# Performance work log

Measured on AMD Instinct MI355X. Metric: run time of the kernel, lower is better.

## Reference

```python
import jax, jax.numpy as jnp
import numpy as np
from jax import lax

LOG2PI = 1.8378770664093453


def _lstm_last(x, Wih, Whh, b, reverse):
    # x: [N, T, D]; returns hidden output at the LAST timestep index (torch output[:, -1])
    N = x.shape[0]
    H = Whh.shape[1]
    xg = jnp.einsum('ntd,gd->tng', x, Wih) + b  # [T, N, 4H], gate order i,f,g,o

    def step(carry, g_in):
        h, c = carry
        g = g_in + h @ Whh.T
        i, f, gg, o = jnp.split(g, 4, axis=-1)
        c = jax.nn.sigmoid(f) * c + jax.nn.sigmoid(i) * jnp.tanh(gg)
        h = jax.nn.sigmoid(o) * jnp.tanh(c)
        return (h, c), h

    init = (jnp.zeros((N, H), x.dtype), jnp.zeros((N, H), x.dtype))
    _, hs = lax.scan(step, init, xg, reverse=reverse)
    return hs[-1]  # fw: full pass; bw(reverse=True): processed only last element, as torch


def _dvbf(x, u, eps1, eps, fw_Wih, fw_Whh, fw_b, bw_Wih, bw_Whh, bw_b,
          i1_w, i1_b, i2_w, i2_b, z1_w, z1_b, z2_w, z2_b,
          wp_w1, wp_b1, wp_w2, wp_b2, vp_w1, vp_b1, vp_w2, vp_b2,
          ob_w1, ob_b1, ob_w2, ob_b2, A, B, C):
    N, T, dx = x.shape
    dw = eps1.shape[1]
    # initial samples from bidirectional LSTM output at t = T-1 (fw || bw)
    h0 = jnp.concatenate([_lstm_last(x, fw_Wih, fw_Whh, fw_b, False),
                          _lstm_last(x, bw_Wih, bw_Whh, bw_b, True)], axis=1)
    p0 = jax.nn.relu(h0 @ i1_w.T + i1_b) @ i2_w.T + i2_b
    m0, s0_raw = jnp.split(p0, 2, axis=1)
    s0 = jnp.exp(s0_raw) + 1e-5
    w1 = m0 + s0 * eps1  # reparameterized torch.normal(mean, std)
    z1 = jax.nn.relu(w1 @ z1_w.T + z1_b) @ z2_w.T + z2_b

    def step(z_t, inp):
        x_t, u_t, e_t = inp
        pw = jnp.tanh(jnp.concatenate([x_t, z_t, u_t], axis=1) @ wp_w1.T + wp_b1) @ wp_w2.T + wp_b2
        m, s_raw = jnp.split(pw, 2, axis=1)
        s = jnp.exp(s_raw) + 0.01
        w_t = m + s * e_t
        alpha = jax.nn.softmax(
            jax.nn.relu(jnp.concatenate([z_t, u_t], axis=1) @ vp_w1.T + vp_b1) @ vp_w2.T + vp_b2,
            axis=1)
        z_n = (jnp.einsum('nm,mij,nj->ni', alpha, A, z_t)
               + jnp.einsum('nm,mij,nj->ni', alpha, B, u_t)
               + jnp.einsum('nm,mij,nj->ni', alpha, C, w_t))
        return z_n, (z_n, m, s)

    xs = (jnp.swapaxes(x[:, 1:], 0, 1), jnp.swapaxes(u[:, :T - 1], 0, 1), jnp.swapaxes(eps[:, 1:], 0, 1))
    _, (zs, ms, ss) = lax.scan(step, z1, xs)
    z = jnp.concatenate([z1[:, None], jnp.swapaxes(zs, 0, 1)], axis=1)        # [N,T,dz]
    w_mean = jnp.concatenate([m0[:, None], jnp.swapaxes(ms, 0, 1)], axis=1)   # [N,T,dw]
    w_std = jnp.concatenate([s0[:, None], jnp.swapaxes(ss, 0, 1)], axis=1)

    x_rec = jax.nn.relu(z @ ob_w1.T + ob_b1) @ ob_w2.T + ob_b2                # [N,T,dx]
    logprob_x = -0.5 * jnp.sum((x - x_rec) ** 2) - 0.5 * N * T * dx * LOG2PI
    # KL(N(m, diag(std)) || N(0, I)) -- the module uses std as the covariance diagonal
    kl = 0.5 * (jnp.sum(w_std) + jnp.sum(w_mean ** 2) - N * T * dw - jnp.sum(jnp.log(w_std)))
    return -(logprob_x - kl)


def setup_inputs() -> dict:
    key = jax.random.key(0)
    ks = iter(jax.random.split(key, 64))

    def rn(shape, s=1.0):
        return s * jax.random.normal(next(ks), shape, dtype=jnp.float32)

    N, T, DX, DU, DZ, DW, M, H = 512, 128, 256, 32, 128, 64, 16, 128
    S = 0.05  # weight scale keeps the recurrence stable
    return {
        'x': rn((N, T, DX)), 'u': rn((N, T, DU)),
        'eps1': rn((N, DW)), 'eps': rn((N, T, DW)),
        'fw_Wih': rn((4 * H, DX), S), 'fw_Whh': rn((4 * H, H), S), 'fw_b': rn((4 * H,), S),
        'bw_Wih': rn((4 * H, DX), S), 'bw_Whh': rn((4 * H, H), S), 'bw_b': rn((4 * H,), S),
        'i1_w': rn((H, 2 * H), S), 'i1_b': rn((H,), S), 'i2_w': rn((2 * DW, H), S), 'i2_b': rn((2 * DW,), S),
        'z1_w': rn((H, DW), S), 'z1_b': rn((H,), S), 'z2_w': rn((DZ, H), S), 'z2_b': rn((DZ,), S),
        'wp_w1': rn((H, DZ + DU + DX), S), 'wp_b1': rn((H,), S), 'wp_w2': rn((2 * DW, H), S), 'wp_b2': rn((2 * DW,), S),
        'vp_w1': rn((H, DZ + DU), S), 'vp_b1': rn((H,), S), 'vp_w2': rn((M, H), S), 'vp_b2': rn((M,), S),
        'ob_w1': rn((H, DZ), S), 'ob_b1': rn((H,), S), 'ob_w2': rn((DX, H), S), 'ob_b2': rn((DX,), S),
        'A': rn((M, DZ, DZ), S), 'B': rn((M, DZ, DU), S), 'C': rn((M, DZ, DW), S),
    }


def reference(x, u, eps1, eps, fw_Wih, fw_Whh, fw_b, bw_Wih, bw_Whh, bw_b,
              i1_w, i1_b, i2_w, i2_b, z1_w, z1_b, z2_w, z2_b,
              wp_w1, wp_b1, wp_w2, wp_b2, vp_w1, vp_b1, vp_w2, vp_b2,
              ob_w1, ob_b1, ob_w2, ob_b2, A, B, C):
    return _dvbf(x, u, eps1, eps, fw_Wih, fw_Whh, fw_b, bw_Wih, bw_Whh, bw_b,
                 i1_w, i1_b, i2_w, i2_b, z1_w, z1_b, z2_w, z2_b,
                 wp_w1, wp_b1, wp_w2, wp_b2, vp_w1, vp_b1, vp_w2, vp_b2,
                 ob_w1, ob_b1, ob_w2, ob_b2, A, B, C)
```

## Files before the change

kernel.cpp:

```cpp
#include <hip/hip_runtime.h>
#include <stdint.h>
#include <math.h>

#define NB  512
#define TT  128
#define DXX 256
#define DUU 32
#define DZZ 128
#define DWW 64
#define MMM 16
#define HHH 128
#define G4  512

typedef __attribute__((ext_vector_type(8))) short bf16x8;
typedef __attribute__((ext_vector_type(4))) float f32x4;
#define MFMA(a,b,c) __builtin_amdgcn_mfma_f32_16x16x32_bf16(a,b,c,0,0,0)
#define MF8(a,b,c)  __builtin_amdgcn_mfma_f32_16x16x32_fp8_fp8(a,b,c,0,0,0)

__device__ __forceinline__ float sigf(float x){ return 1.f/(1.f+__expf(-x)); }
__device__ __forceinline__ float fast_tanh(float x){
    float e = __expf(2.f*x);
    return 1.f - 2.f/(e + 1.f);
}
__device__ __forceinline__ unsigned int f2bf(float f){
// ... 23 lines not shown
        if (rs >= 33) return s;
        uint64_t full = (uint64_t)(mant | 0x800000u);
        uint64_t q = full >> rs;
        uint64_t rem = full & (((uint64_t)1 << rs) - 1);
        uint64_t half = (uint64_t)1 << (rs - 1);
        if (rem > half || (rem == half && (q & 1))) q++;
        code = (uint32_t)q;
    }
    return s | code;
}

__device__ __forceinline__ void stage1k(const void* gsrc, void* ldst, int ln)
{
    __builtin_amdgcn_global_load_lds(
        (const __attribute__((address_space(1))) void*)((const char*)gsrc + ln*16),
        (__attribute__((address_space(3))) void*)ldst, 16, 0, 0);
}
__device__ __forceinline__ void stage32k(const void* gsrc, void* ldst, int tid)
{
    const char* g = (const char*)gsrc;
    char* l = (char*)ldst;
    const int lane = tid & 63;
    const int wv   = tid >> 6;
    #pragma unroll
    for (int it = 0; it < 8; it++){
        const int off = it*4096 + wv*1024;
        __builtin_amdgcn_global_load_lds(
            (const __attribute__((address_space(1))) void*)(g + off + lane*16),
            (__attribute__((address_space(3))) void*)(l + off),
            16, 0, 0);
    }
}

__global__ __launch_bounds__(256) void k_prep2(
    const float* __restrict__ wp_w1, const float* __restrict__ wp_w2,
    const float* __restrict__ vp_w1, const float* __restrict__ vp_w2,
    unsigned short* __restrict__ frag)
{
    const int T = blockIdx.x;
    unsigned short* dst = frag + (size_t)T*512;
    for (int e = threadIdx.x; e < 512; e += 256){
        const int lane = e >> 3, j = e & 7;
        const int m16 = lane & 15, kq = lane >> 4;
        const int kk = 8*kq + j;
        float v = 0.f;
        if (T < 104){
            const int ct = T/13, kt = T%13;
            v = wp_w1[(size_t)(16*ct + m16)*416 + 32*kt + kk];
        } else if (T < 136){
            const int i = T-104, ct = i/4, kt = i%4;
            v = wp_w2[(size_t)(16*ct + m16)*128 + 32*kt + kk];
        } else if (T < 176){
            const int i = T-136, ct = i/5, kt = i%5;
            v = vp_w1[(size_t)(16*ct + m16)*160 + 32*kt + kk];
        } else {
            const int kt = T-176;
            v = vp_w2[(size_t)m16*128 + 32*kt + kk];
        }
        dst[e] = (unsigned short)f2bf(v);
    }
}

__global__ __launch_bounds__(256) void k_prep8(
    const float* __restrict__ Amat, const float* __restrict__ Bmat,
    const float* __restrict__ Cmat, unsigned char* __restrict__ frag8)
{
    const int wv = blockIdx.x >> 3, pair = blockIdx.x & 7;
    unsigned char* dst = frag8 + (size_t)blockIdx.x*7168;
    for (int d = threadIdx.x*4; d < 7168; d += 1024){
        uint32_t pk = 0;
        #pragma unroll
        for (int i = 0; i < 4; i++){
            const int B = d + i;
            const int f = B >> 9, r = B & 511;
            const int lane = r >> 3, jj = r & 7;
            const int m = 2*pair + (f >= 7 ? 1 : 0);
            const int kt = (f >= 7) ? f-7 : f;
            const int col = wv*16 + (lane & 15);
            const int k = kt*32 + (lane >> 4)*8 + jj;
            float v;
            if (k < 128)      v = Amat[((size_t)m*128 + col)*128 + k];
            else if (k < 160) v = Bmat[((size_t)m*128 + col)*32 + (k-128)];
            else              v = Cmat[((size_t)m*128 + col)*64 + (k-160)];
            pk |= f2e4m3(v * 16.f) << (8*i);
        }
        *(uint32_t*)(dst + d) = pk;
    }
}

__global__ __launch_bounds__(256) void k_prep_xg(const float* __restrict__ Wih,
                                                 unsigned short* __restrict__ fragx)
{
    const int T = blockIdx.x;
    const int ct = T >> 3, kt = T & 7;
    unsigned short* dst = fragx + (size_t)T*512;
    for (int e = threadIdx.x; e < 512; e += 256){
        const int lane = e >> 3, j = e & 7;
        const int m16 = lane & 15, kq = lane >> 4;
        const int kk = 8*kq + j;
        float v = Wih[(size_t)(16*ct + m16)*DXX + 32*kt + kk];
        dst[e] = (unsigned short)f2bf(v);
    }
}

__global__ __launch_bounds__(256) void k_prep_lo(
    const float* __restrict__ Whh,
    const float* __restrict__ ob_w1, const float* __restrict__ ob_w2,
    unsigned short* __restrict__ blstm, unsigned short* __restrict__ bob)
{
    const int tile = blockIdx.x;
    unsigned short* dst; int lt;
    if (tile < 4){ dst = blstm + (size_t)tile*16384; lt = 1; }
    else { dst = bob + (size_t)(tile-4)*16384; lt = 2; }
    for (int e = threadIdx.x; e < 16384; e += 256){
        const int g = e >> 7, p = e & 127;
        const int s = p >> 3, j = p & 7;
        const int k = ((s ^ (g & 7)) << 3) | j;
        float v;
        if (lt == 1) v = Whh[(size_t)(tile*128 + g)*128 + k];
        else {
            const int tt = tile - 4;
            if (tt == 0) v = ob_w1[g*128 + k];
            else         v = ob_w2[(size_t)((tt-1)*128 + g)*128 + k];
        }
        dst[e] = (unsigned short)f2bf(v);
    }
}

__global__ __launch_bounds__(256) void k_prep_in(
    const float* __restrict__ X, const float* __restrict__ U, const float* __restrict__ EPS,
    unsigned short* __restrict__ IX, unsigned short* __restrict__ IU,
    unsigned short* __restrict__ IE, unsigned char* __restrict__ IUf)
{
    const int b  = blockIdx.x;
    const int tt = blockIdx.y;
    const int n0 = b*16;
    unsigned short* dx = IX + ((size_t)b*127 + tt)*4096;
    for (int h = threadIdx.x; h < 4096; h += 256){
        const int o = h >> 9, l = (h >> 3) & 63, j = h & 7;
        const int r = 2*o + (l >> 5), v = l & 31;
        const int s = v ^ (r & 7);
        dx[h] = (unsigned short)f2bf(X[((size_t)(n0+r)*TT + tt+1)*DXX + s*8 + j]);
    }
    unsigned short* du = IU + ((size_t)b*127 + tt)*512;
    for (int h = threadIdx.x; h < 512; h += 256){
        const int l = h >> 3, j = h & 7;
        const int r = l >> 2, v = l & 3;
        const int qq = v ^ (r & 3);
        du[h] = (unsigned short)f2bf(U[((size_t)(n0+r)*TT + tt)*DUU + qq*8 + j]);
    }
    unsigned short* de = IE + ((size_t)b*127 + tt)*1024;
    for (int h = threadIdx.x; h < 1024; h += 256){
        const int e2 = h >> 9, l = (h >> 3) & 63, j = h & 7;
        const int r = 8*e2 + (l >> 3);
        de[h] = (unsigned short)f2bf(EPS[((size_t)(n0+r)*TT + tt+1)*DWW + (l&7)*8 + j]);
    }
    unsigned char* df = IUf + ((size_t)b*127 + tt)*512;
    for (int h = threadIdx.x; h < 512; h += 256){
        const int smp = h >> 5, sp = (h >> 3) & 3, j = h & 7;
        const int ud = ((sp ^ (smp & 3))*8) + j;
        df[h] = (unsigned char)f2e4m3(U[((size_t)(n0+smp)*TT + tt)*DUU + ud]);
    }
}

template<int ACT>
__device__ void dense(const float* __restrict__ W, const float* __restrict__ bias,
                      int C, int K, const float* sIn, int ldi,
                      float* sOut, int ldo, float* sWt)
{
    const int tid = threadIdx.x;
    const int g   = tid & 127;
    const int rq  = tid >> 7;
    const int r0  = 2*rq, r1 = 2*rq+1;
    for (int cb = 0; cb < C; cb += 128){
        float acc0 = 0.f, acc1 = 0.f;
        for (int kb = 0; kb < K; kb += 64){
            const int kw = (K - kb < 64) ? (K - kb) : 64;
            __syncthreads();
            if (kw == 64){
                for (int l = tid; l < 128*64; l += 256){
                    int gg = l >> 6, kk = l & 63;
                    int cx = cb + gg;
                    sWt[gg*65 + kk] = (cx < C) ? W[(size_t)cx*K + kb + kk] : 0.f;
                }
            } else {
                for (int l = tid; l < 128*32; l += 256){
                    int gg = l >> 5, kk = l & 31;
                    int cx = cb + gg;
                    sWt[gg*65 + kk] = (cx < C) ? W[(size_t)cx*K + kb + kk] : 0.f;
                }
            }
            __syncthreads();
            const float* ip0 = sIn + r0*ldi + kb;
            const float* ip1 = sIn + r1*ldi + kb;
            const float* wp  = sWt + g*65;
// ... 140 lines not shown
        sH0[r*260+j] = h0[(size_t)(n0+r)*HHH + j];
    }
    dense<0>(bw_Wih, bw_b, 512, 256, sX, 260, sG, 516, sWt);
    __syncthreads();
    for (int l = tid; l < 4*128; l += 256){
        int r = l >> 7, j = l & 127;
        float gi = sG[r*516 + j];
        float gv = sG[r*516 + 256 + j];
        float go = sG[r*516 + 384 + j];
        float c  = sigf(gi)*fast_tanh(gv);
        sH0[r*260 + 128 + j] = sigf(go)*fast_tanh(c);
    }
    dense<1>(i1w, i1b, 128, 256, sH0, 260, sT, 132, sWt);
    dense<0>(i2w, i2b, 128, 128, sT, 132, sP, 132, sWt);
    __syncthreads();
    for (int l = tid; l < 4*64; l += 256){
        int r = l >> 6, j = l & 63;
        float m0 = sP[r*132 + j];
        float s0 = __expf(sP[r*132 + 64 + j]) + 1e-5f;
        float w1 = m0 + s0*eps1[(size_t)(n0+r)*DWW + j];
        wm[((size_t)(n0+r)*TT)*DWW + j]  = m0;
        wsd[((size_t)(n0+r)*TT)*DWW + j] = s0;
        sX[r*68 + j] = w1;
    }
    dense<1>(z1w, z1b, 128, 64, sX, 68, sT, 132, sWt);
    dense<0>(z2w, z2b, 128, 128, sT, 132, sP, 132, sWt);
    __syncthreads();
    for (int l = tid; l < 4*128; l += 256){
        int r = l >> 7, j = l & 127;
        zb[((size_t)(n0+r)*TT)*DZZ + j] = sP[r*132+j];
    }
}

__device__ __forceinline__ int blobIdx(int i, int wv){
    if (i < 13)  return wv*13 + i;
    if (i < 18)  return 136 + wv*5 + (i-13);
    if (i < 22)  return 104 + wv*4 + (i-18);
    if (i < 26)  return 176 + (i-22);
    return 0;
}

#define VWAIT() do{ asm volatile("s_waitcnt vmcnt(7)" ::: "memory"); \
                    __builtin_amdgcn_sched_barrier(0); }while(0)
#define LWAIT() do{ asm volatile("s_waitcnt lgkmcnt(0)" ::: "memory"); \
                    __builtin_amdgcn_sched_barrier(0); }while(0)
#define BAR()   __builtin_amdgcn_s_barrier()

__global__ __launch_bounds__(512) void k_scan(
    const float* __restrict__ wp_b1, const float* __restrict__ wp_b2,
    const float* __restrict__ vp_b1, const float* __restrict__ vp_b2,
    const short* __restrict__ frag, const unsigned char* __restrict__ frag8,
    const unsigned short* __restrict__ IX, const unsigned short* __restrict__ IU,
    const unsigned short* __restrict__ IE, const unsigned char* __restrict__ IUf,
    float* __restrict__ zb, float* __restrict__ wm, float* __restrict__ wsd)
{
    __shared__ __align__(16) short sRing[57344];
    __shared__ __align__(16) short sXr[4096];
    __shared__ __align__(16) short sZr[2048];
    __shared__ __align__(16) short sUr[2][512];
    __shared__ __align__(16) short sEr[1024];
    __shared__ __align__(16) short sH1[2048];
    __shared__ __align__(16) short sH2[2048];
    __shared__ __align__(16) char  sZf[2048];
    __shared__ __align__(16) char  sUf[2][512];
    __shared__ __align__(16) char  sWf[1024];
    __shared__ __align__(16) float sPW[16*132];
    __shared__ __align__(16) float sL [16*20];
    __shared__ float sAl[16*17];

    const int tid = threadIdx.x;
    const int n0  = blockIdx.x * 16;
    const int wv  = tid >> 6;
    const int ln  = tid & 63;
    const int smp = ln & 15, q = ln >> 4;
    const int sx7 = smp & 7;
    char* ringB = (char*)sRing + wv*14336;

    const f32x4 bw1 = *(const f32x4*)&wp_b1[wv*16 + q*4];
    const f32x4 bw2 = *(const f32x4*)&wp_b2[wv*16 + q*4];
    const f32x4 bv1 = *(const f32x4*)&vp_b1[wv*16 + q*4];
    f32x4 bv2 = {0.f,0.f,0.f,0.f};
    if (wv == 0) bv2 = *(const f32x4*)&vp_b2[q*4];

    #define ISSUE_CHUNK(cc_) do{ const int c2_ = (cc_) % 12; \
        if (c2_ < 4){ _Pragma("unroll") \
            for (int k7 = 0; k7 < 7; k7++) \
                stage1k((const char*)frag + (size_t)blobIdx(c2_*7 + k7, wv)*1024, \
                        ringB + (c2_&1)*7168 + k7*1024, ln); \
        } else { _Pragma("unroll") \
            for (int k7 = 0; k7 < 7; k7++) \
                stage1k((const char*)frag8 + (size_t)(wv*8 + (c2_-4))*7168 + k7*1024, \
                        ringB + (c2_&1)*7168 + k7*1024, ln); } }while(0)
    #define AFRAG(gi_)  (*(const bf16x8*)(ringB + (((gi_)/7)&1)*7168 + ((gi_)%7)*1024 + ln*16))
    #define AF8(bf_,f_) (*(const long*)(ringB + (bf_)*7168 + (f_)*512 + ln*8))
    #define BX(kt_)  (*(const bf16x8*)&sXr[smp*256 + (((4*(kt_)+q) ^ sx7)<<3)])
    #define BZ(kz_)  (*(const bf16x8*)&sZr[smp*128 + (((4*(kz_)+q) ^ sx7)<<3)])
    #define BH1(kt_) (*(const bf16x8*)&sH1[smp*128 + (((4*(kt_)+q) ^ sx7)<<3)])
    #define BH2(kt_) (*(const bf16x8*)&sH2[smp*128 + (((4*(kt_)+q) ^ sx7)<<3)])

    auto issue_inputs = [&](int tt){
        const size_t ib = (size_t)blockIdx.x*127 + tt;
        const char* bx8 = (const char*)IX + ib*8192;
        stage1k(bx8 + wv*1024, (char*)sXr + wv*1024, ln);
        if (wv == 0)      stage1k((const char*)IU + ib*1024, (char*)sUr[tt&1], ln);
        else if (wv == 1) stage1k((const char*)IE + ib*2048,        (char*)sEr,        ln);
        else if (wv == 2) stage1k((const char*)IE + ib*2048 + 1024, (char*)sEr + 1024, ln);
        else if (wv == 3){ if (ln < 32) stage1k((const char*)IUf + ib*512, sUf[tt&1], ln); }
    };

    issue_inputs(0);
    if (tid < 256){
        const int zs = tid >> 4, sl = tid & 15;
        const float* zp = &zb[((size_t)(n0+zs)*TT)*DZZ + sl*8];
        float4 a0 = *(const float4*)zp;
        float4 a1 = *(const float4*)(zp+4);
        int4 pk;
        pk.x = f2bf(a0.x) | (f2bf(a0.y)<<16);
        pk.y = f2bf(a0.z) | (f2bf(a0.w)<<16);
        pk.z = f2bf(a1.x) | (f2bf(a1.y)<<16);
        pk.w = f2bf(a1.z) | (f2bf(a1.w)<<16);
        *(int4*)&sZr[zs*128 + ((sl ^ (zs&7))<<3)] = pk;
        uint2 p8;
        p8.x = f2e4m3(a0.x) | (f2e4m3(a0.y)<<8) | (f2e4m3(a0.z)<<16) | (f2e4m3(a0.w)<<24);
        p8.y = f2e4m3(a1.x) | (f2e4m3(a1.y)<<8) | (f2e4m3(a1.z)<<16) | (f2e4m3(a1.w)<<24);
        *(uint2*)&sZf[zs*128 + ((sl ^ (zs&7))<<3)] = p8;
    }
    ISSUE_CHUNK(0);
    ISSUE_CHUNK(1);
    asm volatile("s_waitcnt vmcnt(0)" ::: "memory");
    __builtin_amdgcn_sched_barrier(0);
    LWAIT(); BAR();

    for (int t = 0; t < TT-1; t++){
        const short* sUc = sUr[t&1];
        bf16x8 bu = *(const bf16x8*)&sUc[smp*32 + ((q ^ (sx7&3))<<3)];

        VWAIT();
        f32x4 d1a = {0.f,0.f,0.f,0.f}, d1b = {0.f,0.f,0.f,0.f};
        d1a = MFMA(AFRAG(0), BX(0), d1a); d1b = MFMA(AFRAG(1), BX(1), d1b);
        d1a = MFMA(AFRAG(2), BX(2), d1a); d1b = MFMA(AFRAG(3), BX(3), d1b);
        d1a = MFMA(AFRAG(4), BX(4), d1a); d1b = MFMA(AFRAG(5), BX(5), d1b);
        d1a = MFMA(AFRAG(6), BX(6), d1a);
        ISSUE_CHUNK(2);
        VWAIT();
        d1b = MFMA(AFRAG(7), BX(7), d1b);
        d1a = MFMA(AFRAG(8), BZ(0), d1a); d1b = MFMA(AFRAG(9), BZ(1), d1b);
        d1a = MFMA(AFRAG(10), BZ(2), d1a); d1b = MFMA(AFRAG(11), BZ(3), d1b);
        d1a = MFMA(AFRAG(12), bu, d1a);
        f32x4 d3a = {0.f,0.f,0.f,0.f}, d3b = {0.f,0.f,0.f,0.f};
        d3a = MFMA(AFRAG(13), BZ(0), d3a);
        ISSUE_CHUNK(3);
        VWAIT();
        d3b = MFMA(AFRAG(14), BZ(1), d3b); d3a = MFMA(AFRAG(15), BZ(2), d3a);
        d3b = MFMA(AFRAG(16), BZ(3), d3b); d3a = MFMA(AFRAG(17), bu, d3a);
        bf16x8 aG2a = AFRAG(18), aG2b = AFRAG(19), aG2c = AFRAG(20);
        {
            f32x4 d1 = d1a + d1b, d3 = d3a + d3b;
            float v0 = fast_tanh(d1[0]+bw1[0]);
            float v1 = fast_tanh(d1[1]+bw1[1]);
            float v2 = fast_tanh(d1[2]+bw1[2]);
            float v3 = fast_tanh(d1[3]+bw1[3]);
            const int slot = 2*wv + (q>>1);
            const int baseh = smp*128 + ((slot ^ sx7)<<3) + (q&1)*4;
            *(unsigned int*)&sH1[baseh]   = f2bf(v0) | (f2bf(v1)<<16);
            *(unsigned int*)&sH1[baseh+2] = f2bf(v2) | (f2bf(v3)<<16);
            float w0 = fmaxf(d3[0]+bv1[0], 0.f);
            float w1 = fmaxf(d3[1]+bv1[1], 0.f);
            float w2 = fmaxf(d3[2]+bv1[2], 0.f);
            float w3 = fmaxf(d3[3]+bv1[3], 0.f);
            *(unsigned int*)&sH2[baseh]   = f2bf(w0) | (f2bf(w1)<<16);
            *(unsigned int*)&sH2[baseh+2] = f2bf(w2) | (f2bf(w3)<<16);
        }
        ISSUE_CHUNK(4);
        LWAIT(); BAR();

        VWAIT();
        {
            f32x4 d2a = {0.f,0.f,0.f,0.f}, d2b = {0.f,0.f,0.f,0.f};
            d2a = MFMA(aG2a, BH1(0), d2a); d2b = MFMA(aG2b, BH1(1), d2b);
            d2a = MFMA(aG2c, BH1(2), d2a); d2b = MFMA(AFRAG(21), BH1(3), d2b);
            f32x4 o = d2a + d2b + bw2;
            *(f32x4*)&sPW[smp*132 + wv*16 + q*4] = o;
            if (wv == 0){
                f32x4 d4a = {0.f,0.f,0.f,0.f}, d4b = {0.f,0.f,0.f,0.f};
                d4a = MFMA(AFRAG(22), BH2(0), d4a); d4b = MFMA(AFRAG(23), BH2(1), d4b);
                d4a = MFMA(AFRAG(24), BH2(2), d4a); d4b = MFMA(AFRAG(25), BH2(3), d4b);
                f32x4 o4 = d4a + d4b + bv2;
                *(f32x4*)&sL[smp*20 + q*4] = o4;
            }
        }
        ISSUE_CHUNK(5);
        LWAIT(); BAR();

        {
            const int cs = wv, cj = ln;
            float e0 = bf2f((unsigned short)sEr[cs*64 + cj]);
            float e1 = bf2f((unsigned short)sEr[(cs+8)*64 + cj]);
            float m0 = sPW[cs*132 + cj];
            float s0 = __expf(sPW[cs*132 + 64 + cj]) + 0.01f;
            float m1 = sPW[(cs+8)*132 + cj];
            float s1 = __expf(sPW[(cs+8)*132 + 64 + cj]) + 0.01f;
            float w0 = m0 + s0*e0;
            float w1 = m1 + s1*e1;
            wm [((size_t)(n0+cs  )*TT + t+1)*DWW + cj] = m0;
            wsd[((size_t)(n0+cs  )*TT + t+1)*DWW + cj] = s0;
            wm [((size_t)(n0+cs+8)*TT + t+1)*DWW + cj] = m1;
            wsd[((size_t)(n0+cs+8)*TT + t+1)*DWW + cj] = s1;
            const int sw = cj >> 3;
            sWf[ cs   *64 + ((sw ^ ( cs   &7))<<3) + (cj&7)] = (char)f2e4m3(w0);
            sWf[(cs+8)*64 + ((sw ^ ((cs+8)&7))<<3) + (cj&7)] = (char)f2e4m3(w1);
        }
        if (tid < 16){
            float mx = -1e30f;
            #pragma unroll
            for (int m = 0; m < 16; m++) mx = fmaxf(mx, sL[tid*20+m]);
            float ss = 0.f;
            float ex[16];
            #pragma unroll
            for (int m = 0; m < 16; m++){ ex[m] = __expf(sL[tid*20+m]-mx); ss += ex[m]; }
            float inv = 0.0625f/ss;
            #pragma unroll
            for (int m = 0; m < 16; m++) sAl[tid*17+m] = ex[m]*inv;
        }
        if (t < TT-2) issue_inputs(t+1);
        LWAIT(); BAR();

        long bz0 = *(const long*)&sZf[smp*128 + (((0*4+q) ^ sx7)<<3)];
        long bz1 = *(const long*)&sZf[smp*128 + (((1*4+q) ^ sx7)<<3)];
        long bz2 = *(const long*)&sZf[smp*128 + (((2*4+q) ^ sx7)<<3)];
        long bz3 = *(const long*)&sZf[smp*128 + (((3*4+q) ^ sx7)<<3)];
        long bu8 = *(const long*)&sUf[t&1][smp*32 + ((q ^ (smp&3))<<3)];
        long bw80 = *(const long*)&sWf[smp*64 + ((q ^ sx7)<<3)];
        long bw81 = *(const long*)&sWf[smp*64 + (((4+q) ^ sx7)<<3)];
        f32x4 zac = {0.f,0.f,0.f,0.f};
        #pragma unroll
        for (int j = 0; j < 8; j++){
            const int bf = j & 1;
            VWAIT();
            f32x4 d = {0.f,0.f,0.f,0.f}, e = {0.f,0.f,0.f,0.f};
            d = MF8(AF8(bf,0), bz0, d); e = MF8(AF8(bf,1), bz1, e);
            d = MF8(AF8(bf,2), bz2, d); e = MF8(AF8(bf,3), bz3, e);
            d = MF8(AF8(bf,4), bu8, d); e = MF8(AF8(bf,5), bw80, e);
            d = MF8(AF8(bf,6), bw81, d);
            f32x4 g = {0.f,0.f,0.f,0.f}, h = {0.f,0.f,0.f,0.f};
            g = MF8(AF8(bf,7), bz0, g);  h = MF8(AF8(bf,8), bz1, h);
            g = MF8(AF8(bf,9), bz2, g);  h = MF8(AF8(bf,10), bz3, h);
            g = MF8(AF8(bf,11), bu8, g); h = MF8(AF8(bf,12), bw80, h);
            g = MF8(AF8(bf,13), bw81, g);
            ISSUE_CHUNK(6+j);
            const float al0 = sAl[smp*17 + 2*j];
            const float al1 = sAl[smp*17 + 2*j + 1];
            f32x4 s0 = d + e, s1 = g + h;
            zac[0] += al0*s0[0] + al1*s1[0];
            zac[1] += al0*s0[1] + al1*s1[1];
            zac[2] += al0*s0[2] + al1*s1[2];
            zac[3] += al0*s0[3] + al1*s1[3];
        }
        LWAIT(); BAR();

        {
            const int slotz = 2*wv + (q>>1);
            const int basez = smp*128 + ((slotz ^ sx7)<<3) + (q&1)*4;
            *(unsigned int*)&sZr[basez]   = f2bf(zac[0]) | (f2bf(zac[1])<<16);
            *(unsigned int*)&sZr[basez+2] = f2bf(zac[2]) | (f2bf(zac[3])<<16);
            unsigned int p8 = f2e4m3(zac[0]) | (f2e4m3(zac[1])<<8)
                            | (f2e4m3(zac[2])<<16) | (f2e4m3(zac[3])<<24);
            *(unsigned int*)&sZf[smp*128 + ((slotz ^ sx7)<<3) + (q&1)*4] = p8;
            float4 st = {zac[0], zac[1], zac[2], zac[3]};
            *(float4*)&zb[((size_t)(n0+smp)*TT + t+1)*DZZ + wv*16 + q*4] = st;
        }
        LWAIT(); BAR();
    }
    asm volatile("s_waitcnt vmcnt(0) lgkmcnt(0)" ::: "memory");
    #undef ISSUE_CHUNK
    #undef AFRAG
    #undef AF8
    #undef BX
    #undef BZ
    #undef BH1
    #undef BH2
}

__global__ __launch_bounds__(256) void k_ob(const float* __restrict__ X,
        const float* __restrict__ zb,
        const float* __restrict__ b1, const float* __restrict__ b2,
        const unsigned short* __restrict__ blob, float* __restrict__ acc)
{
    __shared__ __align__(16) char  sW[2][32768];
    __shared__ __align__(16) float sZ[32*128];
    __shared__ __align__(16) float sH[32*128];
    __shared__ float redb[4];
    const int tid = threadIdx.x;
    const size_t row0 = (size_t)blockIdx.x * 32;
    const int g = tid & 127, rh = tid >> 7;
    for (int l = tid; l < 32*128; l += 256)
        sZ[l] = zb[(row0 + (size_t)(l >> 7))*DZZ + (l & 127)];
    stage32k((const char*)blob, sW[0], tid);
    asm volatile("s_waitcnt vmcnt(0)" ::: "memory");
    __syncthreads();
    stage32k((const char*)blob + 32768, sW[1], tid);
    float h[16];
    #pragma unroll
    for (int r = 0; r < 16; r++) h[r] = 0.f;
    #pragma unroll 4
    for (int s = 0; s < 16; s++){
        const uint32_t* wp = (const uint32_t*)(sW[0] + g*256 + ((s ^ (g & 7)) << 4));
        float wv[8];
        #pragma unroll
        for (int d = 0; d < 4; d++){
            uint32_t w2 = wp[d];
            wv[2*d]   = __uint_as_float(w2 << 16);
            wv[2*d+1] = __uint_as_float(w2 & 0xffff0000u);
        }
// ... 114 lines not shown
    const float* i1w = (const float*)d_in[10];
    const float* i1b = (const float*)d_in[11];
    const float* i2w = (const float*)d_in[12];
    const float* i2b = (const float*)d_in[13];
    const float* z1w = (const float*)d_in[14];
    const float* z1b = (const float*)d_in[15];
    const float* z2w = (const float*)d_in[16];
    const float* z2b = (const float*)d_in[17];
    const float* wp_w1 = (const float*)d_in[18];
    const float* wp_b1 = (const float*)d_in[19];
    const float* wp_w2 = (const float*)d_in[20];
    const float* wp_b2 = (const float*)d_in[21];
    const float* vp_w1 = (const float*)d_in[22];
    const float* vp_b1 = (const float*)d_in[23];
    const float* vp_w2 = (const float*)d_in[24];
    const float* vp_b2 = (const float*)d_in[25];
    const float* ob_w1 = (const float*)d_in[26];
    const float* ob_b1 = (const float*)d_in[27];
    const float* ob_w2 = (const float*)d_in[28];
    const float* ob_b2 = (const float*)d_in[29];
    const float* Amat  = (const float*)d_in[30];
    const float* Bmat  = (const float*)d_in[31];
    const float* Cmat  = (const float*)d_in[32];
    float* out = (float*)d_out;

    unsigned short* xgb = (unsigned short*)d_ws;
    float* h0  = (float*)(xgb + (size_t)NB*TT*G4);
    float* zb  = h0  + (size_t)NB*HHH;
    float* wm  = zb  + (size_t)NB*TT*DZZ;
    float* wsd = wm  + (size_t)NB*TT*DWW;
    float* acc = wsd + (size_t)NB*TT*DWW;
    unsigned short* blstm = (unsigned short*)(acc + 64);
    unsigned short* bob   = blstm + (size_t)4*16384;
    unsigned short* bfrag = bob   + (size_t)3*16384;
    unsigned short* bfragx= bfrag + (size_t)180*512;
    unsigned char*  bfrag8= (unsigned char*)(bfragx + (size_t)256*512);
    unsigned short* IX    = (unsigned short*)(bfrag8 + (size_t)64*7168);
    unsigned short* IU    = IX + (size_t)32*127*4096;
    unsigned short* IE    = IU + (size_t)32*127*512;
    unsigned char*  IUf   = (unsigned char*)(IE + (size_t)32*127*1024);

    hipMemsetAsync(acc, 0, 4*sizeof(float), stream);

    k_prep2<<<180, 256, 0, stream>>>(wp_w1, wp_w2, vp_w1, vp_w2, bfrag);
    k_prep8<<<64, 256, 0, stream>>>(Amat, Bmat, Cmat, bfrag8);
    k_prep_xg<<<256, 256, 0, stream>>>(fw_Wih, bfragx);
    k_prep_lo<<<7, 256, 0, stream>>>(fw_Whh, ob_w1, ob_w2, blstm, bob);
    k_prep_in<<<dim3(32,127), 256, 0, stream>>>(x, u, eps, IX, IU, IE, IUf);
    k_xg2 <<<NB*TT/16, 512, 0, stream>>>(x, bfragx, fw_b, xgb);
    k_lstm<<<NB/2, 256, 0, stream>>>(xgb, blstm, h0);
    k_init<<<NB/4, 256, 0, stream>>>(x, bw_Wih, bw_b, i1w, i1b, i2w, i2b,
                                     z1w, z1b, z2w, z2b, eps1, h0, zb, wm, wsd);
    k_scan<<<32, 512, 0, stream>>>(wp_b1, wp_b2, vp_b1, vp_b2,
                                   (const short*)bfrag, bfrag8, IX, IU, IE, IUf,
                                   zb, wm, wsd);
    k_ob  <<<NB*TT/32, 256, 0, stream>>>(x, zb, ob_b1, ob_b2, bob, acc);
    k_kl  <<<NB*TT*DWW/4096, 256, 0, stream>>>(wm, wsd, acc);
    k_final<<<1, 64, 0, stream>>>(acc, out);
}
```

Before: 2.941 ms.

## Precompute x/u projections outside the scan and run all recurrent matmuls in fp8

The input-dependent parts of the first layers of the wp and vp MLPs (x and u terms plus biases) are now computed for every timestep in a new parallel kernel before the scan. The sequential scan keeps only the z-dependent projections, and those, along with the second layers, now use fp8 MFMA with a scaling factor instead of bf16. A single fp8 weight blob per wave is streamed through a larger LDS ring in 8 KB chunks, which removes the bf16/fp8 split and the X staging. The aim is to shorten the serial critical path of the scan. The cost is extra workspace traffic and lower precision in the hidden activations, which are now quantised to e4m3.

```diff
diff --git a/kernel.cpp b/kernel.cpp
--- a/kernel.cpp
+++ b/kernel.cpp
@@ -79,59 +79,56 @@
     }
 }
 
-__global__ __launch_bounds__(256) void k_prep2(
+__global__ __launch_bounds__(256) void k_prep8b(
     const float* __restrict__ wp_w1, const float* __restrict__ wp_w2,
     const float* __restrict__ vp_w1, const float* __restrict__ vp_w2,
-    unsigned short* __restrict__ frag)
-{
-    const int T = blockIdx.x;
-    unsigned short* dst = frag + (size_t)T*512;
+    const float* __restrict__ Amat,  const float* __restrict__ Bmat,
+    const float* __restrict__ Cmat,  unsigned char* __restrict__ frag8)
+{
+    const int wv = blockIdx.x >> 3, c = blockIdx.x & 7;
+    unsigned char* dst = frag8 + (size_t)(wv*8 + c)*8192;
+    for (int d = threadIdx.x*4; d < 8192; d += 1024){
+        uint32_t pk = 0;
+        #pragma unroll
+        for (int i = 0; i < 4; i++){
+            const int B = d + i;
+            const int f = 16*c + (B >> 9), r = B & 511;
+            const int lane = r >> 3, jj = r & 7;
+            const int col = wv*16 + (lane & 15);
+            const int kk = (lane >> 4)*8 + jj;
+            float v = 0.f;
+            if (f < 4)       v = wp_w1[(size_t)col*416 + 256 + f*32 + kk];
+            else if (f < 8)  v = vp_w1[(size_t)col*160 + (f-4)*32 + kk];
+            else if (f < 12) v = wp_w2[(size_t)col*128 + (f-8)*32 + kk];
+            else if (f < 16){ if (wv == 0) v = vp_w2[(size_t)(col&15)*128 + (f-12)*32 + kk]; }
+            else {
+                const int fi = f-16, m = fi/7, kt = fi%7;
+                const int k = kt*32 + kk;
+                if (k < 128)      v = Amat[((size_t)m*128 + col)*128 + k];
+                else if (k < 160) v = Bmat[((size_t)m*128 + col)*32 + (k-128)];
+                else              v = Cmat[((size_t)m*128 + col)*64 + (k-160)];
+            }
+            pk |= f2e4m3(v * 16.f) << (8*i);
+        }
+        *(uint32_t*)(dst + d) = pk;
+    }
+}
+
+__global__ __launch_bounds__(256) void k_prep_p(
+    const float* __restrict__ wp_w1, const float* __restrict__ vp_w1,
+    unsigned short* __restrict__ fragP)
+{
+    const int ct = blockIdx.x / 10, f = blockIdx.x % 10;
+    unsigned short* dst = fragP + (size_t)blockIdx.x*512;
     for (int e = threadIdx.x; e < 512; e += 256){
         const int lane = e >> 3, j = e & 7;
-        const int m16 = lane & 15, kq = lane >> 4;
-        const int kk = 8*kq + j;
-        float v = 0.f;
-        if (T < 104){
-            const int ct = T/13, kt = T%13;
-            v = wp_w1[(size_t)(16*ct + m16)*416 + 32*kt + kk];
-        } else if (T < 136){
-            const int i = T-104, ct = i/4, kt = i%4;
-            v = wp_w2[(size_t)(16*ct + m16)*128 + 32*kt + kk];
-        } else if (T < 176){
-            const int i = T-136, ct = i/5, kt = i%5;
-            v = vp_w1[(size_t)(16*ct + m16)*160 + 32*kt + kk];
-        } else {
-            const int kt = T-176;
-            v = vp_w2[(size_t)m16*128 + 32*kt + kk];
-        }
+        const int col = 16*ct + (lane & 15);
+        const int kk = (lane >> 4)*8 + j;
+        float v;
+        if (f < 8)      v = wp_w1[(size_t)col*416 + f*32 + kk];
+        else if (f == 8) v = wp_w1[(size_t)col*416 + 384 + kk];
+        else             v = vp_w1[(size_t)col*160 + 128 + kk];
         dst[e] = (unsigned short)f2bf(v);
-    }
-}
-
-__global__ __launch_bounds__(256) void k_prep8(
-    const float* __restrict__ Amat, const float* __restrict__ Bmat,
-    const float* __restrict__ Cmat, unsigned char* __restrict__ frag8)
-{
-    const int wv = blockIdx.x >> 3, pair = blockIdx.x & 7;
-    unsigned char* dst = frag8 + (size_t)blockIdx.x*7168;
-    for (int d = threadIdx.x*4; d < 7168; d += 1024){
-        uint32_t pk = 0;
-        #pragma unroll
-        for (int i = 0; i < 4; i++){
-            const int B = d + i;
-            const int f = B >> 9, r = B & 511;
-            const int lane = r >> 3, jj = r & 7;
-            const int m = 2*pair + (f >= 7 ? 1 : 0);
-            const int kt = (f >= 7) ? f-7 : f;
-            const int col = wv*16 + (lane & 15);
-            const int k = kt*32 + (lane >> 4)*8 + jj;
-            float v;
-            if (k < 128)      v = Amat[((size_t)m*128 + col)*128 + k];
-            else if (k < 160) v = Bmat[((size_t)m*128 + col)*32 + (k-128)];
-            else              v = Cmat[((size_t)m*128 + col)*64 + (k-160)];
-            pk |= f2e4m3(v * 16.f) << (8*i);
-        }
-        *(uint32_t*)(dst + d) = pk;
     }
 }
 
@@ -175,27 +172,12 @@
 }
 
 __global__ __launch_bounds__(256) void k_prep_in(
-    const float* __restrict__ X, const float* __restrict__ U, const float* __restrict__ EPS,
-    unsigned short* __restrict__ IX, unsigned short* __restrict__ IU,
+    const float* __restrict__ U, const float* __restrict__ EPS,
     unsigned short* __restrict__ IE, unsigned char* __restrict__ IUf)
 {
     const int b  = blockIdx.x;
     const int tt = blockIdx.y;
     const int n0 = b*16;
-    unsigned short* dx = IX + ((size_t)b*127 + tt)*4096;
-    for (int h = threadIdx.x; h < 4096; h += 256){
-        const int o = h >> 9, l = (h >> 3) & 63, j = h & 7;
-        const int r = 2*o + (l >> 5), v = l & 31;
-        const int s = v ^ (r & 7);
-        dx[h] = (unsigned short)f2bf(X[((size_t)(n0+r)*TT + tt+1)*DXX + s*8 + j]);
-    }
-    unsigned short* du = IU + ((size_t)b*127 + tt)*512;
-    for (int h = threadIdx.x; h < 512; h += 256){
-        const int l = h >> 3, j = h & 7;
-        const int r = l >> 2, v = l & 3;
-        const int qq = v ^ (r & 3);
-        du[h] = (unsigned short)f2bf(U[((size_t)(n0+r)*TT + tt)*DUU + qq*8 + j]);
-    }
     unsigned short* de = IE + ((size_t)b*127 + tt)*1024;
     for (int h = threadIdx.x; h < 1024; h += 256){
         const int e2 = h >> 9, l = (h >> 3) & 63, j = h & 7;
@@ -208,6 +190,65 @@
         const int ud = ((sp ^ (smp & 3))*8) + j;
         df[h] = (unsigned char)f2e4m3(U[((size_t)(n0+smp)*TT + tt)*DUU + ud]);
     }
+}
+
+__global__ __launch_bounds__(512) void k_pxu(
+    const float* __restrict__ X, const float* __restrict__ U,
+    const float* __restrict__ wp_b1, const float* __restrict__ vp_b1,
+    const unsigned short* __restrict__ fragP,
+    unsigned short* __restrict__ IPx, unsigned short* __restrict__ IPL)
+{
+    __shared__ __align__(16) short sXl[16*256];
+    __shared__ __align__(16) short sUl[16*32];
+    const int tid = threadIdx.x;
+    const int b = blockIdx.x, t = blockIdx.y;
+    const int n0 = b*16;
+    const int wv = tid >> 6, ln = tid & 63;
+    const int rr = ln & 15, q = ln >> 4;
+    const int sx7 = rr & 7;
+    {
+        const int r = tid >> 5, sl = tid & 31;
+        const float* xp = &X[((size_t)(n0+r)*TT + t+1)*DXX + sl*8];
+        float4 a0 = *(const float4*)xp;
+        float4 a1 = *(const float4*)(xp+4);
+        int4 pk;
+        pk.x = f2bf(a0.x) | (f2bf(a0.y)<<16);
+        pk.y = f2bf(a0.z) | (f2bf(a0.w)<<16);
+        pk.z = f2bf(a1.x) | (f2bf(a1.y)<<16);
+        pk.w = f2bf(a1.z) | (f2bf(a1.w)<<16);
+        *(int4*)&sXl[r*256 + ((sl ^ (r&7))<<3)] = pk;
+    }
+    {
+        const int r = tid >> 5, cc = tid & 31;
+        sUl[r*32 + (((cc>>3) ^ (r&3))<<3) + (cc&7)] =
+            (unsigned short)f2bf(U[((size_t)(n0+r)*TT + t)*DUU + cc]);
+    }
+    __syncthreads();
+    const short* pA = (const short*)fragP + (size_t)wv*10*512 + ln*8;
+    f32x4 d = {0.f,0.f,0.f,0.f};
+    #pragma unroll
+    for (int kt = 0; kt < 8; kt++){
+        bf16x8 a = *(const bf16x8*)(pA + kt*512);
+        bf16x8 bx = *(const bf16x8*)&sXl[rr*256 + (((4*kt+q) ^ sx7)<<3)];
+        d = MFMA(a, bx, d);
+    }
+    bf16x8 bu = *(const bf16x8*)&sUl[rr*32 + ((q ^ (rr&3))<<3)];
+    d = MFMA(*(const bf16x8*)(pA + 8*512), bu, d);
+    f32x4 dl = {0.f,0.f,0.f,0.f};
+    dl = MFMA(*(const bf16x8*)(pA + 9*512), bu, dl);
+    const f32x4 b1v = *(const f32x4*)&wp_b1[wv*16 + q*4];
+    const f32x4 bLv = *(const f32x4*)&vp_b1[wv*16 + q*4];
+    d = d + b1v;
+    dl = dl + bLv;
+    const size_t base = ((size_t)b*127 + t)*2048
+                      + rr*128 + (((2*wv + (q>>1)) ^ sx7)<<3) + (q&1)*4;
+    uint2 p1, p2;
+    p1.x = f2bf(d[0]) | (f2bf(d[1])<<16);
+    p1.y = f2bf(d[2]) | (f2bf(d[3])<<16);
+    p2.x = f2bf(dl[0]) | (f2bf(dl[1])<<16);
+    p2.y = f2bf(dl[2]) | (f2bf(dl[3])<<16);
+    *(uint2*)&IPx[base] = p1;
+    *(uint2*)&IPL[base] = p2;
 }
 
 template<int ACT>
@@ -414,38 +455,28 @@
     }
 }
 
-__device__ __forceinline__ int blobIdx(int i, int wv){
-    if (i < 13)  return wv*13 + i;
-    if (i < 18)  return 136 + wv*5 + (i-13);
-    if (i < 22)  return 104 + wv*4 + (i-18);
-    if (i < 26)  return 176 + (i-22);
-    return 0;
-}
-
-#define VWAIT() do{ asm volatile("s_waitcnt vmcnt(7)" ::: "memory"); \
+#define VWAIT8() do{ asm volatile("s_waitcnt vmcnt(8)" ::: "memory"); \
                     __builtin_amdgcn_sched_barrier(0); }while(0)
 #define LWAIT() do{ asm volatile("s_waitcnt lgkmcnt(0)" ::: "memory"); \
                     __builtin_amdgcn_sched_barrier(0); }while(0)
 #define BAR()   __builtin_amdgcn_s_barrier()
 
 __global__ __launch_bounds__(512) void k_scan(
-    const float* __restrict__ wp_b1, const float* __restrict__ wp_b2,
-    const float* __restrict__ vp_b1, const float* __restrict__ vp_b2,
-    const short* __restrict__ frag, const unsigned char* __restrict__ frag8,
-    const unsigned short* __restrict__ IX, const unsigned short* __restrict__ IU,
+    const float* __restrict__ wp_b2, const float* __restrict__ vp_b2,
+    const unsigned char* __restrict__ frag8,
+    const unsigned short* __restrict__ IPx, const unsigned short* __restrict__ IPL,
     const unsigned short* __restrict__ IE, const unsigned char* __restrict__ IUf,
     float* __restrict__ zb, float* __restrict__ wm, float* __restrict__ wsd)
 {
-    __shared__ __align__(16) short sRing[57344];
-    __shared__ __align__(16) short sXr[4096];
-    __shared__ __align__(16) short sZr[2048];
-    __shared__ __align__(16) short sUr[2][512];
-    __shared__ __align__(16) short sEr[1024];
-    __shared__ __align__(16) short sH1[2048];
-    __shared__ __align__(16) short sH2[2048];
+    __shared__ __align__(16) short sRing[65536];
+    __shared__ __align__(16) short sPx[2048];
+    __shared__ __align__(16) short sPL[2048];
     __shared__ __align__(16) char  sZf[2048];
     __shared__ __align__(16) char  sUf[2][512];
     __shared__ __align__(16) char  sWf[1024];
+    __shared__ __align__(16) short sEr[1024];
+    __shared__ __align__(16) char  sH1f[2048];
+    __shared__ __align__(16) char  sH2f[2048];
     __shared__ __align__(16) float sPW[16*132];
     __shared__ __align__(16) float sL [16*20];
     __shared__ float sAl[16*17];
@@ -456,38 +487,29 @@
     const int ln  = tid & 63;
     const int smp = ln & 15, q = ln >> 4;
     const int sx7 = smp & 7;
-    char* ringB = (char*)sRing + wv*14336;
-
-    const f32x4 bw1 = *(const f32x4*)&wp_b1[wv*16 + q*4];
+    char* ringB = (char*)sRing + wv*16384;
+    const unsigned char* myblob = frag8 + (size_t)wv*65536;
+
     const f32x4 bw2 = *(const f32x4*)&wp_b2[wv*16 + q*4];
-    const f32x4 bv1 = *(const f32x4*)&vp_b1[wv*16 + q*4];
     f32x4 bv2 = {0.f,0.f,0.f,0.f};
     if (wv == 0) bv2 = *(const f32x4*)&vp_b2[q*4];
 
-    #define ISSUE_CHUNK(cc_) do{ const int c2_ = (cc_) % 12; \
-        if (c2_ < 4){ _Pragma("unroll") \
-            for (int k7 = 0; k7 < 7; k7++) \
-                stage1k((const char*)frag + (size_t)blobIdx(c2_*7 + k7, wv)*1024, \
-                        ringB + (c2_&1)*7168 + k7*1024, ln); \
-        } else { _Pragma("unroll") \
-            for (int k7 = 0; k7 < 7; k7++) \
-                stage1k((const char*)frag8 + (size_t)(wv*8 + (c2_-4))*7168 + k7*1024, \
-                        ringB + (c2_&1)*7168 + k7*1024, ln); } }while(0)
-    #define AFRAG(gi_)  (*(const bf16x8*)(ringB + (((gi_)/7)&1)*7168 + ((gi_)%7)*1024 + ln*16))
-    #define AF8(bf_,f_) (*(const long*)(ringB + (bf_)*7168 + (f_)*512 + ln*8))
-    #define BX(kt_)  (*(const bf16x8*)&sXr[smp*256 + (((4*(kt_)+q) ^ sx7)<<3)])
-    #define BZ(kz_)  (*(const bf16x8*)&sZr[smp*128 + (((4*(kz_)+q) ^ sx7)<<3)])
-    #define BH1(kt_) (*(const bf16x8*)&sH1[smp*128 + (((4*(kt_)+q) ^ sx7)<<3)])
-    #define BH2(kt_) (*(const bf16x8*)&sH2[smp*128 + (((4*(kt_)+q) ^ sx7)<<3)])
+    #define ISSUE_CHUNK(cc_) do{ const int c2_ = (cc_) & 7; \
+        _Pragma("unroll") \
+        for (int k8 = 0; k8 < 8; k8++) \
+            stage1k(myblob + (size_t)c2_*8192 + k8*1024, \
+                    ringB + (c2_&1)*8192 + k8*1024, ln); }while(0)
+    #define AF8(f_) (*(const long*)(ringB + (((f_)>>4)&1)*8192 + ((f_)&15)*512 + ln*8))
+    #define BH1F(t_) (*(const long*)&sH1f[smp*128 + (((4*(t_)+q) ^ sx7)<<3)])
+    #define BH2F(t_) (*(const long*)&sH2f[smp*128 + (((4*(t_)+q) ^ sx7)<<3)])
 
     auto issue_inputs = [&](int tt){
         const size_t ib = (size_t)blockIdx.x*127 + tt;
-        const char* bx8 = (const char*)IX + ib*8192;
-        stage1k(bx8 + wv*1024, (char*)sXr + wv*1024, ln);
-        if (wv == 0)      stage1k((const char*)IU + ib*1024, (char*)sUr[tt&1], ln);
-        else if (wv == 1) stage1k((const char*)IE + ib*2048,        (char*)sEr,        ln);
-        else if (wv == 2) stage1k((const char*)IE + ib*2048 + 1024, (char*)sEr + 1024, ln);
-        else if (wv == 3){ if (ln < 32) stage1k((const char*)IUf + ib*512, sUf[tt&1], ln); }
+        if (wv < 4) stage1k((const char*)IPx + ib*4096 + wv*1024, (char*)sPx + wv*1024, ln);
+        else        stage1k((const char*)IPL + ib*4096 + (wv-4)*1024, (char*)sPL + (wv-4)*1024, ln);
+        if (wv == 0)      stage1k((const char*)IE + ib*2048,        (char*)sEr,        ln);
+        else if (wv == 1) stage1k((const char*)IE + ib*2048 + 1024, (char*)sEr + 1024, ln);
+        else if (wv == 2){ if (ln < 32) stage1k((const char*)IUf + ib*512, sUf[tt&1], ln); }
     };
 
     issue_inputs(0);
@@ -496,12 +518,6 @@
         const float* zp = &zb[((size_t)(n0+zs)*TT)*DZZ + sl*8];
         float4 a0 = *(const float4*)zp;
         float4 a1 = *(const float4*)(zp+4);
-        int4 pk;
-        pk.x = f2bf(a0.x) | (f2bf(a0.y)<<16);
-        pk.y = f2bf(a0.z) | (f2bf(a0.w)<<16);
-        pk.z = f2bf(a1.x) | (f2bf(a1.y)<<16);
-        pk.w = f2bf(a1.z) | (f2bf(a1.w)<<16);
-        *(int4*)&sZr[zs*128 + ((sl ^ (zs&7))<<3)] = pk;
         uint2 p8;
         p8.x = f2e4m3(a0.x) | (f2e4m3(a0.y)<<8) | (f2e4m3(a0.z)<<16) | (f2e4m3(a0.w)<<24);
         p8.y = f2e4m3(a1.x) | (f2e4m3(a1.y)<<8) | (f2e4m3(a1.z)<<16) | (f2e4m3(a1.w)<<24);
@@ -514,64 +530,57 @@
     LWAIT(); BAR();
 
     for (int t = 0; t < TT-1; t++){
-        const short* sUc = sUr[t&1];
-        bf16x8 bu = *(const bf16x8*)&sUc[smp*32 + ((q ^ (sx7&3))<<3)];
-
-        VWAIT();
+        long bz0 = *(const long*)&sZf[smp*128 + (((0*4+q) ^ sx7)<<3)];
+        long bz1 = *(const long*)&sZf[smp*128 + (((1*4+q) ^ sx7)<<3)];
+        long bz2 = *(const long*)&sZf[smp*128 + (((2*4+q) ^ sx7)<<3)];
+        long bz3 = *(const long*)&sZf[smp*128 + (((3*4+q) ^ sx7)<<3)];
+
+        VWAIT8();
         f32x4 d1a = {0.f,0.f,0.f,0.f}, d1b = {0.f,0.f,0.f,0.f};
-        d1a = MFMA(AFRAG(0), BX(0), d1a); d1b = MFMA(AFRAG(1), BX(1), d1b);
-        d1a = MFMA(AFRAG(2), BX(2), d1a); d1b = MFMA(AFRAG(3), BX(3), d1b);
-        d1a = MFMA(AFRAG(4), BX(4), d1a); d1b = MFMA(AFRAG(5), BX(5), d1b);
-        d1a = MFMA(AFRAG(6), BX(6), d1a);
+        d1a = MF8(AF8(0), bz0, d1a); d1b = MF8(AF8(1), bz1, d1b);
+        d1a = MF8(AF8(2), bz2, d1a); d1b = MF8(AF8(3), bz3, d1b);
+        f32x4 d3a = {0.f,0.f,0.f,0.f}, d3b = {0.f,0.f,0.f,0.f};
+        d3a = MF8(AF8(4), bz0, d3a); d3b = MF8(AF8(5), bz1, d3b);
+        d3a = MF8(AF8(6), bz2, d3a); d3b = MF8(AF8(7), bz3, d3b);
+        long aG2_0 = AF8(8),  aG2_1 = AF8(9),  aG2_2 = AF8(10), aG2_3 = AF8(11);
+        long aG4_0 = AF8(12), aG4_1 = AF8(13), aG4_2 = AF8(14), aG4_3 = AF8(15);
+        LWAIT();
         ISSUE_CHUNK(2);
-        VWAIT();
-        d1b = MFMA(AFRAG(7), BX(7), d1b);
-        d1a = MFMA(AFRAG(8), BZ(0), d1a); d1b = MFMA(AFRAG(9), BZ(1), d1b);
-        d1a = MFMA(AFRAG(10), BZ(2), d1a); d1b = MFMA(AFRAG(11), BZ(3), d1b);
-        d1a = MFMA(AFRAG(12), bu, d1a);
-        f32x4 d3a = {0.f,0.f,0.f,0.f}, d3b = {0.f,0.f,0.f,0.f};
-        d3a = MFMA(AFRAG(13), BZ(0), d3a);
-        ISSUE_CHUNK(3);
-        VWAIT();
-        d3b = MFMA(AFRAG(14), BZ(1), d3b); d3a = MFMA(AFRAG(15), BZ(2), d3a);
-        d3b = MFMA(AFRAG(16), BZ(3), d3b); d3a = MFMA(AFRAG(17), bu, d3a);
-        bf16x8 aG2a = AFRAG(18), aG2b = AFRAG(19), aG2c = AFRAG(20);
         {
+            const int basep = smp*128 + (((2*wv + (q>>1)) ^ sx7)<<3) + (q&1)*4;
+            uint2 pxw = *(const uint2*)&sPx[basep];
+            uint2 plw = *(const uint2*)&sPL[basep];
             f32x4 d1 = d1a + d1b, d3 = d3a + d3b;
-            float v0 = fast_tanh(d1[0]+bw1[0]);
-            float v1 = fast_tanh(d1[1]+bw1[1]);
-            float v2 = fast_tanh(d1[2]+bw1[2]);
-            float v3 = fast_tanh(d1[3]+bw1[3]);
-            const int slot = 2*wv + (q>>1);
-            const int baseh = smp*128 + ((slot ^ sx7)<<3) + (q&1)*4;
-            *(unsigned int*)&sH1[baseh]   = f2bf(v0) | (f2bf(v1)<<16);
-            *(unsigned int*)&sH1[baseh+2] = f2bf(v2) | (f2bf(v3)<<16);
-            float w0 = fmaxf(d3[0]+bv1[0], 0.f);
-            float w1 = fmaxf(d3[1]+bv1[1], 0.f);
-            float w2 = fmaxf(d3[2]+bv1[2], 0.f);
-            float w3 = fmaxf(d3[3]+bv1[3], 0.f);
-            *(unsigned int*)&sH2[baseh]   = f2bf(w0) | (f2bf(w1)<<16);
-            *(unsigned int*)&sH2[baseh+2] = f2bf(w2) | (f2bf(w3)<<16);
-        }
-        ISSUE_CHUNK(4);
+            float v0 = fast_tanh(d1[0]*0.0625f + bf2f((unsigned short)(pxw.x & 0xffff)));
+            float v1 = fast_tanh(d1[1]*0.0625f + bf2f((unsigned short)(pxw.x >> 16)));
+            float v2 = fast_tanh(d1[2]*0.0625f + bf2f((unsigned short)(pxw.y & 0xffff)));
+            float v3 = fast_tanh(d1[3]*0.0625f + bf2f((unsigned short)(pxw.y >> 16)));
+            const int baseh = smp*128 + (((2*wv + (q>>1)) ^ sx7)<<3) + (q&1)*4;
+            *(unsigned int*)&sH1f[baseh] =
+                f2e4m3(v0) | (f2e4m3(v1)<<8) | (f2e4m3(v2)<<16) | (f2e4m3(v3)<<24);
+            float w0 = fmaxf(d3[0]*0.0625f + bf2f((unsigned short)(plw.x & 0xffff)), 0.f);
+            float w1 = fmaxf(d3[1]*0.0625f + bf2f((unsigned short)(plw.x >> 16)), 0.f);
+            float w2 = fmaxf(d3[2]*0.0625f + bf2f((unsigned short)(plw.y & 0xffff)), 0.f);
+            float w3 = fmaxf(d3[3]*0.0625f + bf2f((unsigned short)(plw.y >> 16)), 0.f);
+            *(unsigned int*)&sH2f[baseh] =
+                f2e4m3(w0) | (f2e4m3(w1)<<8) | (f2e4m3(w2)<<16) | (f2e4m3(w3)<<24);
+        }
         LWAIT(); BAR();
 
-        VWAIT();
         {
             f32x4 d2a = {0.f,0.f,0.f,0.f}, d2b = {0.f,0.f,0.f,0.f};
-            d2a = MFMA(aG2a, BH1(0), d2a); d2b = MFMA(aG2b, BH1(1), d2b);
-            d2a = MFMA(aG2c, BH1(2), d2a); d2b = MFMA(AFRAG(21), BH1(3), d2b);
-            f32x4 o = d2a + d2b + bw2;
+            d2a = MF8(aG2_0, BH1F(0), d2a); d2b = MF8(aG2_1, BH1F(1), d2b);
+            d2a = MF8(aG2_2, BH1F(2), d2a); d2b = MF8(aG2_3, BH1F(3), d2b);
+            f32x4 o = (d2a + d2b)*0.0625f + bw2;
             *(f32x4*)&sPW[smp*132 + wv*16 + q*4] = o;
             if (wv == 0){
                 f32x4 d4a = {0.f,0.f,0.f,0.f}, d4b = {0.f,0.f,0.f,0.f};
-                d4a = MFMA(AFRAG(22), BH2(0), d4a); d4b = MFMA(AFRAG(23), BH2(1), d4b);
-                d4a = MFMA(AFRAG(24), BH2(2), d4a); d4b = MFMA(AFRAG(25), BH2(3), d4b);
-                f32x4 o4 = d4a + d4b + bv2;
+                d4a = MF8(aG4_0, BH2F(0), d4a); d4b = MF8(aG4_1, BH2F(1), d4b);
+                d4a = MF8(aG4_2, BH2F(2), d4a); d4b = MF8(aG4_3, BH2F(3), d4b);
+                f32x4 o4 = (d4a + d4b)*0.0625f + bv2;
                 *(f32x4*)&sL[smp*20 + q*4] = o4;
             }
         }
-        ISSUE_CHUNK(5);
         LWAIT(); BAR();
 
         {
@@ -607,44 +616,44 @@
         if (t < TT-2) issue_inputs(t+1);
         LWAIT(); BAR();
 
-        long bz0 = *(const long*)&sZf[smp*128 + (((0*4+q) ^ sx7)<<3)];
-        long bz1 = *(const long*)&sZf[smp*128 + (((1*4+q) ^ sx7)<<3)];
-        long bz2 = *(const long*)&sZf[smp*128 + (((2*4+q) ^ sx7)<<3)];
-        long bz3 = *(const long*)&sZf[smp*128 + (((3*4+q) ^ sx7)<<3)];
         long bu8 = *(const long*)&sUf[t&1][smp*32 + ((q ^ (smp&3))<<3)];
         long bw80 = *(const long*)&sWf[smp*64 + ((q ^ sx7)<<3)];
         long bw81 = *(const long*)&sWf[smp*64 + (((4+q) ^ sx7)<<3)];
         f32x4 zac = {0.f,0.f,0.f,0.f};
-        #pragma unroll
-        for (int j = 0; j < 8; j++){
-            const int bf = j & 1;
-            VWAIT();
-            f32x4 d = {0.f,0.f,0.f,0.f}, e = {0.f,0.f,0.f,0.f};
-            d = MF8(AF8(bf,0), bz0, d); e = MF8(AF8(bf,1), bz1, e);
-            d = MF8(AF8(bf,2), bz2, d); e = MF8(AF8(bf,3), bz3, e);
-            d = MF8(AF8(bf,4), bu8, d); e = MF8(AF8(bf,5), bw80, e);
-            d = MF8(AF8(bf,6), bw81, d);
-            f32x4 g = {0.f,0.f,0.f,0.f}, h = {0.f,0.f,0.f,0.f};
-            g = MF8(AF8(bf,7), bz0, g);  h = MF8(AF8(bf,8), bz1, h);
-            g = MF8(AF8(bf,9), bz2, g);  h = MF8(AF8(bf,10), bz3, h);
-            g = MF8(AF8(bf,11), bu8, g); h = MF8(AF8(bf,12), bw80, h);
-            g = MF8(AF8(bf,13), bw81, g);
-            ISSUE_CHUNK(6+j);
-            const float al0 = sAl[smp*17 + 2*j];
-            const float al1 = sAl[smp*17 + 2*j + 1];
-            f32x4 s0 = d + e, s1 = g + h;
-            zac[0] += al0*s0[0] + al1*s1[0];
-            zac[1] += al0*s0[1] + al1*s1[1];
-            zac[2] += al0*s0[2] + al1*s1[2];
-            zac[3] += al0*s0[3] + al1*s1[3];
+        f32x4 da = {0.f,0.f,0.f,0.f}, db = {0.f,0.f,0.f,0.f};
+        #pragma unroll
+        for (int c = 1; c <= 7; c++){
+            VWAIT8();
+            #pragma unroll
+            for (int pos = 0; pos < 16; pos++){
+                const int fi = 16*(c-1) + pos;
+                const int m  = fi/7, kt = fi%7;
+                long a = AF8(16*c + pos);
+                long b;
+                if (kt == 0) b = bz0;
+                else if (kt == 1) b = bz1;
+                else if (kt == 2) b = bz2;
+                else if (kt == 3) b = bz3;
+                else if (kt == 4) b = bu8;
+                else if (kt == 5) b = bw80;
+                else b = bw81;
+                if (kt & 1) db = MF8(a, b, db);
+                else        da = MF8(a, b, da);
+                if (kt == 6){
+                    const float al = sAl[smp*17 + m];
+                    f32x4 s = da + db;
+                    zac[0] += al*s[0]; zac[1] += al*s[1];
+                    zac[2] += al*s[2]; zac[3] += al*s[3];
+                    da = (f32x4){0.f,0.f,0.f,0.f};
+                    db = (f32x4){0.f,0.f,0.f,0.f};
+                }
+            }
+            ISSUE_CHUNK(c+2);
         }
         LWAIT(); BAR();
 
         {
             const int slotz = 2*wv + (q>>1);
-            const int basez = smp*128 + ((slotz ^ sx7)<<3) + (q&1)*4;
-            *(unsigned int*)&sZr[basez]   = f2bf(zac[0]) | (f2bf(zac[1])<<16);
-            *(unsigned int*)&sZr[basez+2] = f2bf(zac[2]) | (f2bf(zac[3])<<16);
             unsigned int p8 = f2e4m3(zac[0]) | (f2e4m3(zac[1])<<8)
                             | (f2e4m3(zac[2])<<16) | (f2e4m3(zac[3])<<24);
             *(unsigned int*)&sZf[smp*128 + ((slotz ^ sx7)<<3) + (q&1)*4] = p8;
@@ -655,12 +664,9 @@
     }
     asm volatile("s_waitcnt vmcnt(0) lgkmcnt(0)" ::: "memory");
     #undef ISSUE_CHUNK
-    #undef AFRAG
     #undef AF8
-    #undef BX
-    #undef BZ
-    #undef BH1
-    #undef BH2
+    #undef BH1F
+    #undef BH2F
 }
 
 __global__ __launch_bounds__(256) void k_ob(const float* __restrict__ X,
@@ -841,27 +847,28 @@
     float* acc = wsd + (size_t)NB*TT*DWW;
     unsigned short* blstm = (unsigned short*)(acc + 64);
     unsigned short* bob   = blstm + (size_t)4*16384;
-    unsigned short* bfrag = bob   + (size_t)3*16384;
-    unsigned short* bfragx= bfrag + (size_t)180*512;
-    unsigned char*  bfrag8= (unsigned char*)(bfragx + (size_t)256*512);
-    unsigned short* IX    = (unsigned short*)(bfrag8 + (size_t)64*7168);
-    unsigned short* IU    = IX + (size_t)32*127*4096;
-    unsigned short* IE    = IU + (size_t)32*127*512;
+    unsigned short* bfragx= bob   + (size_t)3*16384;
+    unsigned short* fragP = bfragx+ (size_t)256*512;
+    unsigned char*  frag8 = (unsigned char*)(fragP + (size_t)80*512);
+    unsigned short* IPx   = (unsigned short*)(frag8 + (size_t)8*65536);
+    unsigned short* IPL   = IPx + (size_t)32*127*2048;
+    unsigned short* IE    = IPL + (size_t)32*127*2048;
     unsigned char*  IUf   = (unsigned char*)(IE + (size_t)32*127*1024);
 
     hipMemsetAsync(acc, 0, 4*sizeof(float), stream);
 
-    k_prep2<<<180, 256, 0, stream>>>(wp_w1, wp_w2, vp_w1, vp_w2, bfrag);
-    k_prep8<<<64, 256, 0, stream>>>(Amat, Bmat, Cmat, bfrag8);
+    k_prep8b<<<64, 256, 0, stream>>>(wp_w1, wp_w2, vp_w1, vp_w2,
+                                     Amat, Bmat, Cmat, frag8);
+    k_prep_p<<<80, 256, 0, stream>>>(wp_w1, vp_w1, fragP);
     k_prep_xg<<<256, 256, 0, stream>>>(fw_Wih, bfragx);
     k_prep_lo<<<7, 256, 0, stream>>>(fw_Whh, ob_w1, ob_w2, blstm, bob);
-    k_prep_in<<<dim3(32,127), 256, 0, stream>>>(x, u, eps, IX, IU, IE, IUf);
+    k_prep_in<<<dim3(32,127), 256, 0, stream>>>(u, eps, IE, IUf);
+    k_pxu <<<dim3(32,127), 512, 0, stream>>>(x, u, wp_b1, vp_b1, fragP, IPx, IPL);
     k_xg2 <<<NB*TT/16, 512, 0, stream>>>(x, bfragx, fw_b, xgb);
     k_lstm<<<NB/2, 256, 0, stream>>>(xgb, blstm, h0);
     k_init<<<NB/4, 256, 0, stream>>>(x, bw_Wih, bw_b, i1w, i1b, i2w, i2b,
                                      z1w, z1b, z2w, z2b, eps1, h0, zb, wm, wsd);
-    k_scan<<<32, 512, 0, stream>>>(wp_b1, wp_b2, vp_b1, vp_b2,
-                                   (const short*)bfrag, bfrag8, IX, IU, IE, IUf,
+    k_scan<<<32, 512, 0, stream>>>(wp_b2, vp_b2, frag8, IPx, IPL, IE, IUf,
                                    zb, wm, wsd);
     k_ob  <<<NB*TT/32, 256, 0, stream>>>(x, zb, ob_b1, ob_b2, bob, acc);
     k_kl  <<<NB*TT*DWW/4096, 256, 0, stream>>>(wm, wsd, acc);
```

After: 2.852 ms. -3.0%, faster.
